# Kernel tuning notes

Measured on AMD Instinct MI355X. Metric: run time of the kernel, lower is better.

## Reference

```python
import jax, jax.numpy as jnp
import numpy as np

N = 50000      # nodes
E = 800000     # edges (avg degree 16)
F0 = 128       # input features
F = 128        # per-layer out_features (layer output = 2F after alpha/beta concat)
M = 16         # n_machines
BN_EPS = 1e-3  # Keras BatchNormalization default epsilon


def setup_inputs() -> dict:
    key = jax.random.key(0)
    ks = jax.random.split(key, 12)
    x = jax.random.normal(ks[0], (N, F0), jnp.float32)
    adj_rows = jax.random.randint(ks[1], (E,), 0, N, jnp.int32)
    adj_cols = jax.random.randint(ks[2], (E,), 0, N, jnp.int32)
    adj_vals = jax.random.uniform(ks[3], (E,), jnp.float32)
    l0_Walpha = jax.random.normal(ks[4], (6, F0, F), jnp.float32) * 0.05
    l0_Wbeta = jax.random.normal(ks[5], (6, F0, F), jnp.float32) * 0.05
    l0_bn = jax.random.normal(ks[6], (4, F), jnp.float32)
    l1_Walpha = jax.random.normal(ks[7], (6, 2 * F, F), jnp.float32) * 0.05
    l1_Wbeta = jax.random.normal(ks[8], (6, 2 * F, F), jnp.float32) * 0.05
    l1_bn = jax.random.normal(ks[9], (4, F), jnp.float32)
    We = jax.random.normal(ks[10], (2 * F, M), jnp.float32) * 0.05
    be = jax.random.normal(ks[11], (M,), jnp.float32) * 0.05
    return dict(x=x, adj_rows=adj_rows, adj_cols=adj_cols, adj_vals=adj_vals,
                l0_Walpha=l0_Walpha, l0_Wbeta=l0_Wbeta, l0_bn=l0_bn,
                l1_Walpha=l1_Walpha, l1_Wbeta=l1_Wbeta, l1_bn=l1_bn,
                We=We, be=be)


def _spmm(rows, cols, vals, x):
    # y[r] = sum_{edges (r,c)} vals * x[c]  == sparse A @ x
    return jax.ops.segment_sum(vals[:, None] * x[cols], rows, num_segments=x.shape[0])


def _bn(h, gamma, beta):
    # Keras BatchNormalization(axis=1) on (N, F): per-feature stats over nodes (training mode)
    mu = jnp.mean(h, axis=0, keepdims=True)
    var = jnp.var(h, axis=0, keepdims=True)
    return gamma * (h - mu) * jax.lax.rsqrt(var + BN_EPS) + beta


def _gnn_layer(x, rows, cols, vals, Wa, Wb, bn):
    a0 = _spmm(rows, cols, vals, x)
    a1 = _spmm(rows, cols, vals, a0)
    a2 = _spmm(rows, cols, vals, _spmm(rows, cols, vals, a1))
    alpha = x @ (Wa[0] + Wa[1] + Wa[2]) + a0 @ Wa[3] + a1 @ Wa[4] + a2 @ Wa[5]
    alpha = _bn(jax.nn.relu(alpha), bn[0], bn[1])
    beta = x @ (Wb[0] + Wb[1] + Wb[2]) + a0 @ Wb[3] + a1 @ Wb[4] + a2 @ Wb[5]
    beta = _bn(beta, bn[2], bn[3])
    return jnp.concatenate((alpha, beta), axis=1)  # (N, 2F)


def reference(x, adj_rows, adj_cols, adj_vals,
              l0_Walpha, l0_Wbeta, l0_bn,
              l1_Walpha, l1_Wbeta, l1_bn,
              We, be):
    h = _gnn_layer(x, adj_rows, adj_cols, adj_vals, l0_Walpha, l0_Wbeta, l0_bn)
    h = _gnn_layer(h, adj_rows, adj_cols, adj_vals, l1_Walpha, l1_Wbeta, l1_bn)
    # EdgeDense: per-edge score per machine = adj_val * (z[row] + z[col])
    z = h @ We + be                                   # (N, M)
    scores = adj_vals[:, None] * (z[adj_rows] + z[adj_cols])  # (E, M)
    return jax.nn.softmax(scores, axis=1)
```

## Files before the change

### kernel.cpp

```cpp
#include <hip/hip_runtime.h>
#include <stdint.h>

#define NN 50000
#define NE 800000
#define NP 50048
#define SCANB 196

typedef _Float16 f16x8 __attribute__((ext_vector_type(8)));
typedef float f32x4 __attribute__((ext_vector_type(4)));

__device__ __forceinline__ float h2f(unsigned short u){
  union { unsigned short u; _Float16 h; } x; x.u = u; return (float)x.h;
}
__device__ __forceinline__ unsigned short f2h(float f){
  union { _Float16 h; unsigned short u; } x; x.h = (_Float16)f; return x.u;
}
__device__ __forceinline__ void load_lds16(const void* g, void* l){
  __builtin_amdgcn_global_load_lds((const __attribute__((address_space(1))) void*)g,
                                   (__attribute__((address_space(3))) void*)l, 16, 0, 0);
}

__global__ void k_cast(const float* __restrict__ src, unsigned short* __restrict__ dst, int n4){
  int i = blockIdx.x*blockDim.x + threadIdx.x;
  if (i >= n4) return;
  float4 v = ((const float4*)src)[i];
  uint2 o;
  o.x = (unsigned int)f2h(v.x) | ((unsigned int)f2h(v.y) << 16);
  o.y = (unsigned int)f2h(v.z) | ((unsigned int)f2h(v.w) << 16);
  ((uint2*)dst)[i] = o;
}

__global__ void k_hist(const int* __restrict__ rows, int* __restrict__ cnt){
  int e = blockIdx.x*blockDim.x + threadIdx.x;
  if (e < NE) atomicAdd(&cnt[rows[e]], 1);
}

__global__ void k_scan1(const int* __restrict__ cnt, int* __restrict__ rowptr, int* __restrict__ bsum){
  __shared__ int sh[256];
  int t = threadIdx.x, b = blockIdx.x;
  int idx = b * 256 + t;
  int v = (idx < NN) ? cnt[idx] : 0;
  sh[t] = v; __syncthreads();
  #pragma unroll
  for (int off = 1; off < 256; off <<= 1){
    int u = (t >= off) ? sh[t - off] : 0;
    __syncthreads();
    sh[t] += u;
    __syncthreads();
  }
  if (idx < NN) rowptr[idx] = sh[t] - v;
  if (t == 255) bsum[b] = sh[255];
}

__global__ void k_scan3(int* __restrict__ rowptr, const int* __restrict__ bsum){
  __shared__ int sh[256];
  int t = threadIdx.x, b = blockIdx.x;
  int v = (t < SCANB) ? bsum[t] : 0;
  sh[t] = v; __syncthreads();
  #pragma unroll
  for (int off = 1; off < 256; off <<= 1){
    int u = (t >= off) ? sh[t - off] : 0;
    __syncthreads();
    sh[t] += u;
    __syncthreads();
  }
  int boffb = (b == 0) ? 0 : sh[b - 1];
  int total = sh[SCANB - 1];
  int idx = b * 256 + t;
  if (idx < NN) rowptr[idx] += boffb;
  else if (idx == NN) rowptr[NN] = total;
}

__global__ void k_scatter(const int* __restrict__ rows, const int* __restrict__ cols,
                          const float* __restrict__ vals,
                          const int* __restrict__ rowptr, int* __restrict__ fill,
                          int* __restrict__ colss, float* __restrict__ valss){
  int e = blockIdx.x*blockDim.x + threadIdx.x;
  if (e >= NE) return;
  int r = rows[e];
  int p = rowptr[r] + atomicAdd(&fill[r], 1);
  colss[p] = cols[e];
  valss[p] = vals[e];
}

__global__ void k_buildWT(const float* __restrict__ Wa, const float* __restrict__ Wb,
                          unsigned short* __restrict__ WT, int Fin){
  int Ktot = 4 * Fin;
  int idx = blockIdx.x*blockDim.x + threadIdx.x;
  if (idx >= 256 * Ktot) return;
  int j = idx / Ktot, k = idx - j * Ktot;
  int seg = k / Fin, ki = k - seg * Fin;
  const float* W = (j < 128) ? Wa : Wb;
  int jj = (j < 128) ? j : j - 128;
  int stride = Fin * 128;
  float v;
  if (seg == 0)
    v = W[0*stride + ki*128 + jj] + W[1*stride + ki*128 + jj] + W[2*stride + ki*128 + jj];
  else
    v = W[(seg + 2)*stride + ki*128 + jj];
  WT[j*Ktot + k] = f2h(v);
}

template<int F>
__global__ void k_spmm(const int* __restrict__ rowptr, const int* __restrict__ colss,
                       const float* __restrict__ valss,
                       const unsigned short* __restrict__ X, unsigned short* __restrict__ Y){
  int row = blockIdx.x * (blockDim.x >> 6) + (threadIdx.x >> 6);
  if (row >= NN) return;
  int lane = threadIdx.x & 63;
  constexpr int P = F / 64;
  float acc[P];
  #pragma unroll
  for (int i = 0; i < P; i++) acc[i] = 0.f;
  int s = rowptr[row], e = rowptr[row + 1];
  for (int base = s; base < e; base += 64){
    int idx = base + lane;
    bool ok = idx < e;
    int   cc = ok ? colss[idx] : 0;
    float vv = ok ? valss[idx] : 0.f;
    int n = e - base; if (n > 64) n = 64;
    int nr = (n + 15) & ~15;
    for (int jb = 0; jb < nr; jb += 16){
      int cj[16]; float vj[16];
      #pragma unroll
      for (int u = 0; u < 16; u++){
        cj[u] = __shfl(cc, jb + u);
        vj[u] = __shfl(vv, jb + u);
      }
      if (P == 2){
        unsigned int g[16];
        #pragma unroll
        for (int u = 0; u < 16; u++)
          g[u] = *(const unsigned int*)(X + (size_t)cj[u] * F + lane * P);
        #pragma unroll
        for (int u = 0; u < 16; u++){
          acc[0] += vj[u] * h2f((unsigned short)g[u]);
          acc[1] += vj[u] * h2f((unsigned short)(g[u] >> 16));
        }
      } else {
        uint2 g[16];
        #pragma unroll
        for (int u = 0; u < 16; u++)
          g[u] = *(const uint2*)(X + (size_t)cj[u] * F + lane * P);
        #pragma unroll
        for (int u = 0; u < 16; u++){
          acc[0] += vj[u] * h2f((unsigned short)g[u].x);
          acc[1] += vj[u] * h2f((unsigned short)(g[u].x >> 16));
          acc[2] += vj[u] * h2f((unsigned short)g[u].y);
          acc[3] += vj[u] * h2f((unsigned short)(g[u].y >> 16));
        }
      }
    }
  }
  unsigned short* dst = Y + (size_t)row * F + lane * P;
  if (P == 2){
    unsigned int o = (unsigned int)f2h(acc[0]) | ((unsigned int)f2h(acc[1]) << 16);
    *(unsigned int*)dst = o;
  } else {
    uint2 o;
    o.x = (unsigned int)f2h(acc[0]) | ((unsigned int)f2h(acc[1]) << 16);
    o.y = (unsigned int)f2h(acc[2]) | ((unsigned int)f2h(acc[3]) << 16);
    *(uint2*)dst = o;
  }
}

template<int FIN>
__global__ __launch_bounds__(256) void k_gemm4(
    const unsigned short* __restrict__ A0, const unsigned short* __restrict__ A1,
    const unsigned short* __restrict__ A2, const unsigned short* __restrict__ A3,
    const unsigned short* __restrict__ BT, unsigned short* __restrict__ Hp,
    float* __restrict__ stats){
  constexpr int KTOT = 4 * FIN;
  __shared__ unsigned short As[128 * 32];
  __shared__ unsigned short Bs[128 * 32];
  int tid = threadIdx.x, lane = tid & 63;
  int wm = (tid >> 6) & 1, wn = tid >> 7;
  int bm = blockIdx.x, bn = blockIdx.y;

  f32x4 acc[4][4];
  #pragma unroll
  for (int i = 0; i < 4; i++)
    #pragma unroll
    for (int j = 0; j < 4; j++) acc[i][j] = (f32x4){0.f, 0.f, 0.f, 0.f};

  int ac = (tid & 3) * 8;
  int gr0 = bm * 128 + (tid >> 2);        if (gr0 >= NN) gr0 = NN - 1;
  int gr1 = bm * 128 + ((256 + tid) >> 2); if (gr1 >= NN) gr1 = NN - 1;
  int br0 = (tid >> 2), br1 = ((256 + tid) >> 2);
  const unsigned short* Bb = BT + (size_t)(bn * 128) * KTOT;
  unsigned short* Adst0 = As + (size_t)(tid & ~63) * 8;
  unsigned short* Adst1 = As + (size_t)(256 + (tid & ~63)) * 8;
  unsigned short* Bdst0 = Bs + (size_t)(tid & ~63) * 8;
  unsigned short* Bdst1 = Bs + (size_t)(256 + (tid & ~63)) * 8;

  int m0 = wm * 64 + (lane & 15);
  int n0 = wn * 64 + (lane & 15);
  int qk = (lane >> 4) * 8;

  #pragma unroll
  for (int seg = 0; seg < 4; seg++){
    const unsigned short* Asrc = (seg == 0) ? A0 : (seg == 1) ? A1 : (seg == 2) ? A2 : A3;
    const unsigned short* Bseg = Bb + seg * FIN;
    for (int kl = 0; kl < FIN; kl += 32){
      load_lds16(Asrc + (size_t)gr0 * FIN + kl + ac, Adst0);
      load_lds16(Asrc + (size_t)gr1 * FIN + kl + ac, Adst1);
      load_lds16(Bseg + (size_t)br0 * KTOT + kl + ac, Bdst0);
      load_lds16(Bseg + (size_t)br1 * KTOT + kl + ac, Bdst1);
      __syncthreads();
      f16x8 af[4], bfr[4];
      #pragma unroll
      for (int i = 0; i < 4; i++) af[i]  = *(const f16x8*)(As + (m0 + i * 16) * 32 + qk);
      #pragma unroll
      for (int j = 0; j < 4; j++) bfr[j] = *(const f16x8*)(Bs + (n0 + j * 16) * 32 + qk);
      #pragma unroll
      for (int i = 0; i < 4; i++)
        #pragma unroll
        for (int j = 0; j < 4; j++)
          acc[i][j] = __builtin_amdgcn_mfma_f32_16x16x32_f16(af[i], bfr[j], acc[i][j], 0, 0, 0);
      __syncthreads();
    }
  }
  int cnb = bn * 128 + wn * 64 + (lane & 15);
  int rb  = bm * 128 + wm * 64 + ((lane >> 4) << 2);
  float sj[4], qj[4];
  #pragma unroll
  for (int j = 0; j < 4; j++){
    float sv = 0.f, qv = 0.f;
    #pragma unroll
    for (int i = 0; i < 4; i++)
      #pragma unroll
      for (int g = 0; g < 4; g++){
        int rr = rb + i * 16 + g;
        float val = acc[i][j][g];
        bool okr = rr < NN;
        if (okr) Hp[(size_t)rr * 256 + cnb + j * 16] = f2h(val);
        float v = okr ? val : 0.f;
        if (bn == 0) v = fmaxf(v, 0.f);
        sv += v; qv += v * v;
      }
    sj[j] = sv; qj[j] = qv;
  }
  #pragma unroll
  for (int j = 0; j < 4; j++){
    sj[j] += __shfl_xor(sj[j], 16); sj[j] += __shfl_xor(sj[j], 32);
    qj[j] += __shfl_xor(qj[j], 16); qj[j] += __shfl_xor(qj[j], 32);
  }
  if (lane < 16){
    #pragma unroll
    for (int j = 0; j < 4; j++){
      int c = bn * 128 + wn * 64 + j * 16 + lane;
      atomicAdd(&stats[c], sj[j]);
      atomicAdd(&stats[256 + c], qj[j]);
    }
  }
}

__global__ void k_bnapply(const unsigned short* __restrict__ Hp, const float* __restrict__ stats,
                          const float* __restrict__ bnp, unsigned short* __restrict__ OUT){
  __shared__ float scs[256], sbs[256];
  int t = threadIdx.x;
  {
    const float invN = 1.f / (float)NN;
    float mu = stats[t] * invN;
    float var = stats[256 + t] * invN - mu * mu;
    int jj = (t < 128) ? t : t - 128;
    float g = bnp[(t < 128 ? 0 : 2) * 128 + jj];
    float b = bnp[(t < 128 ? 1 : 3) * 128 + jj];
    float sc = g * rsqrtf(var + 1e-3f);
    scs[t] = sc; sbs[t] = b - mu * sc;
  }
  __syncthreads();
  float sc = scs[t], sh = sbs[t];
  for (int r = blockIdx.x; r < NN; r += gridDim.x){
    float v = h2f(Hp[(size_t)r * 256 + t]);
    if (t < 128) v = fmaxf(v, 0.f);
    OUT[(size_t)r * 256 + t] = f2h(v * sc + sh);
  }
}

__global__ void k_bnzdense(const unsigned short* __restrict__ Hp, const float* __restrict__ stats,
                           const float* __restrict__ bnp,
                           const float* __restrict__ We, const float* __restrict__ be,
                           float* __restrict__ Z){
  __shared__ float Hs[16 * 256];
  __shared__ float Ws[256 * 16];
  __shared__ float scs[256], sbs[256];
  int t = threadIdx.x;
  {
    const float invN = 1.f / (float)NN;
    float mu = stats[t] * invN;
    float var = stats[256 + t] * invN - mu * mu;
    int jj = (t < 128) ? t : t - 128;
    float g = bnp[(t < 128 ? 0 : 2) * 128 + jj];
    float b = bnp[(t < 128 ? 1 : 3) * 128 + jj];
    float sc = g * rsqrtf(var + 1e-3f);
    scs[t] = sc; sbs[t] = b - mu * sc;
  }
  __syncthreads();
  int r0 = blockIdx.x * 16;
  for (int i = t; i < 4096; i += 256){
    int col = i & 255;
    float v = h2f(Hp[(size_t)r0 * 256 + i]);
    if (col < 128) v = fmaxf(v, 0.f);
    Hs[i] = v * scs[col] + sbs[col];
    Ws[i] = We[i];
  }
  __syncthreads();
  int r = t >> 4, m = t & 15;
  float accv = be[m];
  const float* hrow = Hs + r * 256;
  #pragma unroll 8
  for (int k = 0; k < 256; k++) accv += hrow[k] * Ws[k * 16 + m];
  Z[(size_t)(r0 + r) * 16 + m] = accv;
}

__global__ void k_edge(const int* __restrict__ rows, const int* __restrict__ cols,
                       const float* __restrict__ vals, const float* __restrict__ Z,
                       float* __restrict__ out){
  int e = blockIdx.x * blockDim.x + threadIdx.x;
  if (e >= NE) return;
  int r = rows[e], c = cols[e];
  float v = vals[e];
  const float4* zr = (const float4*)(Z + (size_t)r * 16);
  const float4* zc = (const float4*)(Z + (size_t)c * 16);
  float s[16];
  #pragma unroll
  for (int q = 0; q < 4; q++){
    float4 a = zr[q], b = zc[q];
    s[q * 4 + 0] = v * (a.x + b.x);
    s[q * 4 + 1] = v * (a.y + b.y);
    s[q * 4 + 2] = v * (a.z + b.z);
    s[q * 4 + 3] = v * (a.w + b.w);
  }
  float mx = s[0];
  #pragma unroll
  for (int i = 1; i < 16; i++) mx = fmaxf(mx, s[i]);
  float sum = 0.f;
  #pragma unroll
  for (int i = 0; i < 16; i++){ s[i] = __expf(s[i] - mx); sum += s[i]; }
  float inv = 1.f / sum;
  float4* po = (float4*)(out + (size_t)e * 16);
  #pragma unroll
  for (int q = 0; q < 4; q++)
    po[q] = make_float4(s[q*4+0]*inv, s[q*4+1]*inv, s[q*4+2]*inv, s[q*4+3]*inv);
}

extern "C" void kernel_launch(void* const* d_in, const int* in_sizes, int n_in,
                              void* d_out, int out_size, void* d_ws, size_t ws_size,
                              hipStream_t stream){
  const float* x    = (const float*)d_in[0];
  const int* rows   = (const int*)d_in[1];
  const int* cols   = (const int*)d_in[2];
  const float* vals = (const float*)d_in[3];
  const float* l0Wa = (const float*)d_in[4];
  const float* l0Wb = (const float*)d_in[5];
  const float* l0bn = (const float*)d_in[6];
  const float* l1Wa = (const float*)d_in[7];
  const float* l1Wb = (const float*)d_in[8];
  const float* l1bn = (const float*)d_in[9];
  const float* We   = (const float*)d_in[10];
  const float* be   = (const float*)d_in[11];
  float* out        = (float*)d_out;

  uint8_t* p = (uint8_t*)d_ws;
  auto take = [&](size_t b) -> void* { void* q = (void*)p; p += (b + 255) & ~(size_t)255; return q; };
  int*   rowptr = (int*)take((size_t)(NN + 1) * 4);
  int*   cnt    = (int*)take((size_t)NN * 4);
  int*   fill   = (int*)take((size_t)NN * 4);
  int*   bsum   = (int*)take((size_t)SCANB * 4);
  int*   colss  = (int*)take((size_t)NE * 4);
  float* valss  = (float*)take((size_t)NE * 4);
  unsigned short* WT0 = (unsigned short*)take((size_t)256 * 512 * 2);
  unsigned short* WT1 = (unsigned short*)take((size_t)256 * 1024 * 2);
  float* stats  = (float*)take(512 * 4);
  float* Z      = (float*)take((size_t)NN * 16 * 4);
  unsigned short* Hp  = (unsigned short*)take((size_t)NN * 256 * 2);
  unsigned short* x16 = (unsigned short*)take((size_t)NN * 128 * 2);
  unsigned short* buf[5];
  for (int i = 0; i < 5; i++) buf[i] = (unsigned short*)take((size_t)NN * 256 * 2);

  hipMemsetAsync(cnt, 0, (size_t)NN * 4, stream);
  hipMemsetAsync(fill, 0, (size_t)NN * 4, stream);
  k_hist<<<NE / 256, 256, 0, stream>>>(rows, cnt);
  k_scan1<<<SCANB, 256, 0, stream>>>(cnt, rowptr, bsum);
  k_scan3<<<SCANB, 256, 0, stream>>>(rowptr, bsum);
  k_scatter<<<NE / 256, 256, 0, stream>>>(rows, cols, vals, rowptr, fill, colss, valss);
  k_buildWT<<<(256 * 512) / 256, 256, 0, stream>>>(l0Wa, l0Wb, WT0, 128);
  k_buildWT<<<(256 * 1024) / 256, 256, 0, stream>>>(l1Wa, l1Wb, WT1, 256);
  k_cast<<<(NN * 128 / 4 + 255) / 256, 256, 0, stream>>>(x, x16, NN * 128 / 4);

  dim3 gg(NP / 128, 2);

  k_spmm<128><<<NN / 4, 256, 0, stream>>>(rowptr, colss, valss, x16,    buf[0]);
  k_spmm<128><<<NN / 4, 256, 0, stream>>>(rowptr, colss, valss, buf[0], buf[1]);
  k_spmm<128><<<NN / 4, 256, 0, stream>>>(rowptr, colss, valss, buf[1], buf[2]);
  k_spmm<128><<<NN / 4, 256, 0, stream>>>(rowptr, colss, valss, buf[2], buf[3]);
  hipMemsetAsync(stats, 0, 512 * 4, stream);
  k_gemm4<128><<<gg, 256, 0, stream>>>(x16, buf[0], buf[1], buf[3], WT0, Hp, stats);
  k_bnapply<<<2048, 256, 0, stream>>>(Hp, stats, l0bn, buf[4]);

  k_spmm<256><<<NN / 4, 256, 0, stream>>>(rowptr, colss, valss, buf[4], buf[0]);
  k_spmm<256><<<NN / 4, 256, 0, stream>>>(rowptr, colss, valss, buf[0], buf[1]);
  k_spmm<256><<<NN / 4, 256, 0, stream>>>(rowptr, colss, valss, buf[1], buf[2]);
  k_spmm<256><<<NN / 4, 256, 0, stream>>>(rowptr, colss, valss, buf[2], buf[3]);
  hipMemsetAsync(stats, 0, 512 * 4, stream);
  k_gemm4<256><<<gg, 256, 0, stream>>>(buf[4], buf[0], buf[1], buf[3], WT1, Hp, stats);
  k_bnzdense<<<NN / 16, 256, 0, stream>>>(Hp, stats, l1bn, We, be, Z);

  k_edge<<<NE / 256, 256, 0, stream>>>(rows, cols, vals, Z, out);
}
```

Before: 758.4 us.

## Split wide SpMM rows across two wavefronts and move BN stats to separate kernel

```diff
diff --git a/kernel.cpp b/kernel.cpp
--- a/kernel.cpp
+++ b/kernel.cpp
@@ -101,17 +101,18 @@
   WT[j*Ktot + k] = f2h(v);
 }
 
-template<int F>
+template<int XS>
 __global__ void k_spmm(const int* __restrict__ rowptr, const int* __restrict__ colss,
                        const float* __restrict__ valss,
                        const unsigned short* __restrict__ X, unsigned short* __restrict__ Y){
-  int row = blockIdx.x * (blockDim.x >> 6) + (threadIdx.x >> 6);
+  constexpr int SEC = XS / 128;
+  int gw = blockIdx.x * 4 + (threadIdx.x >> 6);
+  int row = gw / SEC;
+  int sec = gw - row * SEC;
   if (row >= NN) return;
   int lane = threadIdx.x & 63;
-  constexpr int P = F / 64;
-  float acc[P];
-  #pragma unroll
-  for (int i = 0; i < P; i++) acc[i] = 0.f;
+  const unsigned short* Xb = X + sec * 128 + lane * 2;
+  float acc0 = 0.f, acc1 = 0.f;
   int s = rowptr[row], e = rowptr[row + 1];
   for (int base = s; base < e; base += 64){
     int idx = base + lane;
@@ -127,49 +128,26 @@
         cj[u] = __shfl(cc, jb + u);
         vj[u] = __shfl(vv, jb + u);
       }
-      if (P == 2){
-        unsigned int g[16];
-        #pragma unroll
-        for (int u = 0; u < 16; u++)
-          g[u] = *(const unsigned int*)(X + (size_t)cj[u] * F + lane * P);
-        #pragma unroll
-        for (int u = 0; u < 16; u++){
-          acc[0] += vj[u] * h2f((unsigned short)g[u]);
-          acc[1] += vj[u] * h2f((unsigned short)(g[u] >> 16));
-        }
-      } else {
-        uint2 g[16];
-        #pragma unroll
-        for (int u = 0; u < 16; u++)
-          g[u] = *(const uint2*)(X + (size_t)cj[u] * F + lane * P);
-        #pragma unroll
-        for (int u = 0; u < 16; u++){
-          acc[0] += vj[u] * h2f((unsigned short)g[u].x);
-          acc[1] += vj[u] * h2f((unsigned short)(g[u].x >> 16));
-          acc[2] += vj[u] * h2f((unsigned short)g[u].y);
-          acc[3] += vj[u] * h2f((unsigned short)(g[u].y >> 16));
-        }
+      unsigned int g[16];
+      #pragma unroll
+      for (int u = 0; u < 16; u++)
+        g[u] = *(const unsigned int*)(Xb + (size_t)cj[u] * XS);
+      #pragma unroll
+      for (int u = 0; u < 16; u++){
+        acc0 += vj[u] * h2f((unsigned short)g[u]);
+        acc1 += vj[u] * h2f((unsigned short)(g[u] >> 16));
       }
     }
   }
-  unsigned short* dst = Y + (size_t)row * F + lane * P;
-  if (P == 2){
-    unsigned int o = (unsigned int)f2h(acc[0]) | ((unsigned int)f2h(acc[1]) << 16);
-    *(unsigned int*)dst = o;
-  } else {
-    uint2 o;
-    o.x = (unsigned int)f2h(acc[0]) | ((unsigned int)f2h(acc[1]) << 16);
-    o.y = (unsigned int)f2h(acc[2]) | ((unsigned int)f2h(acc[3]) << 16);
-    *(uint2*)dst = o;
-  }
+  unsigned int o = (unsigned int)f2h(acc0) | ((unsigned int)f2h(acc1) << 16);
+  *(unsigned int*)(Y + (size_t)row * XS + sec * 128 + lane * 2) = o;
 }
 
 template<int FIN>
 __global__ __launch_bounds__(256) void k_gemm4(
     const unsigned short* __restrict__ A0, const unsigned short* __restrict__ A1,
     const unsigned short* __restrict__ A2, const unsigned short* __restrict__ A3,
-    const unsigned short* __restrict__ BT, unsigned short* __restrict__ Hp,
-    float* __restrict__ stats){
+    const unsigned short* __restrict__ BT, unsigned short* __restrict__ Hp){
   constexpr int KTOT = 4 * FIN;
   __shared__ unsigned short As[128 * 32];
   __shared__ unsigned short Bs[128 * 32];
@@ -220,39 +198,29 @@
       __syncthreads();
     }
   }
-  int cnb = bn * 128 + wn * 64 + (lane & 15);
-  int rb  = bm * 128 + wm * 64 + ((lane >> 4) << 2);
-  float sj[4], qj[4];
-  #pragma unroll
-  for (int j = 0; j < 4; j++){
-    float sv = 0.f, qv = 0.f;
+  int cn = bn * 128 + wn * 64 + (lane & 15);
+  int rb = bm * 128 + wm * 64 + ((lane >> 4) << 2);
+  #pragma unroll
+  for (int i = 0; i < 4; i++)
     #pragma unroll
-    for (int i = 0; i < 4; i++)
+    for (int j = 0; j < 4; j++)
       #pragma unroll
       for (int g = 0; g < 4; g++){
         int rr = rb + i * 16 + g;
-        float val = acc[i][j][g];
-        bool okr = rr < NN;
-        if (okr) Hp[(size_t)rr * 256 + cnb + j * 16] = f2h(val);
-        float v = okr ? val : 0.f;
-        if (bn == 0) v = fmaxf(v, 0.f);
-        sv += v; qv += v * v;
+        if (rr < NN) Hp[(size_t)rr * 256 + cn + j * 16] = f2h(acc[i][j][g]);
       }
-    sj[j] = sv; qj[j] = qv;
-  }
-  #pragma unroll
-  for (int j = 0; j < 4; j++){
-    sj[j] += __shfl_xor(sj[j], 16); sj[j] += __shfl_xor(sj[j], 32);
-    qj[j] += __shfl_xor(qj[j], 16); qj[j] += __shfl_xor(qj[j], 32);
-  }
-  if (lane < 16){
-    #pragma unroll
-    for (int j = 0; j < 4; j++){
-      int c = bn * 128 + wn * 64 + j * 16 + lane;
-      atomicAdd(&stats[c], sj[j]);
-      atomicAdd(&stats[256 + c], qj[j]);
-    }
-  }
+}
+
+__global__ void k_bnstats(const unsigned short* __restrict__ Hp, float* __restrict__ stats){
+  int j = threadIdx.x;
+  float s = 0.f, s2 = 0.f;
+  for (int r = blockIdx.x; r < NN; r += gridDim.x){
+    float v = h2f(Hp[(size_t)r * 256 + j]);
+    if (j < 128) v = fmaxf(v, 0.f);
+    s += v; s2 += v * v;
+  }
+  atomicAdd(&stats[j], s);
+  atomicAdd(&stats[256 + j], s2);
 }
 
 __global__ void k_bnapply(const unsigned short* __restrict__ Hp, const float* __restrict__ stats,
@@ -390,21 +358,25 @@
   k_cast<<<(NN * 128 / 4 + 255) / 256, 256, 0, stream>>>(x, x16, NN * 128 / 4);
 
   dim3 gg(NP / 128, 2);
-
-  k_spmm<128><<<NN / 4, 256, 0, stream>>>(rowptr, colss, valss, x16,    buf[0]);
-  k_spmm<128><<<NN / 4, 256, 0, stream>>>(rowptr, colss, valss, buf[0], buf[1]);
-  k_spmm<128><<<NN / 4, 256, 0, stream>>>(rowptr, colss, valss, buf[1], buf[2]);
-  k_spmm<128><<<NN / 4, 256, 0, stream>>>(rowptr, colss, valss, buf[2], buf[3]);
+  const int g128 = (NN + 3) / 4;
+  const int g256 = (NN * 2 + 3) / 4;
+
+  k_spmm<128><<<g128, 256, 0, stream>>>(rowptr, colss, valss, x16,    buf[0]);
+  k_spmm<128><<<g128, 256, 0, stream>>>(rowptr, colss, valss, buf[0], buf[1]);
+  k_spmm<128><<<g128, 256, 0, stream>>>(rowptr, colss, valss, buf[1], buf[2]);
+  k_spmm<128><<<g128, 256, 0, stream>>>(rowptr, colss, valss, buf[2], buf[3]);
+  k_gemm4<128><<<gg, 256, 0, stream>>>(x16, buf[0], buf[1], buf[3], WT0, Hp);
   hipMemsetAsync(stats, 0, 512 * 4, stream);
-  k_gemm4<128><<<gg, 256, 0, stream>>>(x16, buf[0], buf[1], buf[3], WT0, Hp, stats);
+  k_bnstats<<<512, 256, 0, stream>>>(Hp, stats);
   k_bnapply<<<2048, 256, 0, stream>>>(Hp, stats, l0bn, buf[4]);
 
-  k_spmm<256><<<NN / 4, 256, 0, stream>>>(rowptr, colss, valss, buf[4], buf[0]);
-  k_spmm<256><<<NN / 4, 256, 0, stream>>>(rowptr, colss, valss, buf[0], buf[1]);
-  k_spmm<256><<<NN / 4, 256, 0, stream>>>(rowptr, colss, valss, buf[1], buf[2]);
-  k_spmm<256><<<NN / 4, 256, 0, stream>>>(rowptr, colss, valss, buf[2], buf[3]);
+  k_spmm<256><<<g256, 256, 0, stream>>>(rowptr, colss, valss, buf[4], buf[0]);
+  k_spmm<256><<<g256, 256, 0, stream>>>(rowptr, colss, valss, buf[0], buf[1]);
+  k_spmm<256><<<g256, 256, 0, stream>>>(rowptr, colss, valss, buf[1], buf[2]);
+  k_spmm<256><<<g256, 256, 0, stream>>>(rowptr, colss, valss, buf[2], buf[3]);
+  k_gemm4<256><<<gg, 256, 0, stream>>>(buf[4], buf[0], buf[1], buf[3], WT1, Hp);
   hipMemsetAsync(stats, 0, 512 * 4, stream);
-  k_gemm4<256><<<gg, 256, 0, stream>>>(buf[4], buf[0], buf[1], buf[3], WT1, Hp, stats);
+  k_bnstats<<<512, 256, 0, stream>>>(Hp, stats);
   k_bnzdense<<<NN / 16, 256, 0, stream>>>(Hp, stats, l1bn, We, be, Z);
 
   k_edge<<<NE / 256, 256, 0, stream>>>(rows, cols, vals, Z, out);
```

After: 793.0 us. 4.6% more time.
